# Kernel optimization log

Measured on AMD Instinct MI355X. Metric: run time of the kernel, lower is better.

The kernel has to match this reference:

```python
import jax, jax.numpy as jnp
import numpy as np

VOCAB = 38
EMB = 128
CTX = 5  # context window size
HIDDEN = [512, 256, 128]


def setup_inputs() -> dict:
    key = jax.random.key(0)
    ks = jax.random.split(key, 16)
    B, S = 64, 1024
    encrypted_input = jax.random.randint(ks[0], (B, S), 0, VOCAB, dtype=jnp.int32)
    # embedding table, uniform(-0.1, 0.1), padding_idx=0 row zeroed
    emb = jax.random.uniform(ks[1], (VOCAB, EMB), jnp.float32, -0.1, 0.1)
    emb = emb.at[0].set(0.0)
    dims = [EMB * CTX] + HIDDEN + [VOCAB]
    params = {}
    for i in range(len(dims) - 1):
        fan_in, fan_out = dims[i], dims[i + 1]
        limit = float(np.sqrt(6.0 / (fan_in + fan_out)))  # xavier uniform
        params[f"W{i+1}"] = jax.random.uniform(ks[2 + i], (fan_out, fan_in), jnp.float32, -limit, limit)
        params[f"b{i+1}"] = jnp.zeros((fan_out,), jnp.float32)
    return {"encrypted_input": encrypted_input, "emb": emb, **params}


def reference(encrypted_input, emb, W1, b1, W2, b2, W3, b3, W4, b4):
    B, S = encrypted_input.shape
    pad = CTX // 2
    x = emb[encrypted_input]                                   # [B, S, E]
    xp = jnp.pad(x, ((0, 0), (pad, pad), (0, 0)))              # [B, S+4, E]
    # sliding window of CTX tokens, flattened -> [B, S, CTX*E]
    ctx = jnp.concatenate([xp[:, i:i + S, :] for i in range(CTX)], axis=-1)
    h = ctx.reshape(B * S, CTX * EMB)                          # fused batched GEMM rows
    h = jax.nn.relu(h @ W1.T + b1)
    h = jax.nn.relu(h @ W2.T + b2)
    h = jax.nn.relu(h @ W3.T + b3)
    out = h @ W4.T + b4                                        # [B*S, VOCAB]
    return out.reshape(B, S, VOCAB)
```

## Files before the change

### kernel.cpp

```cpp
#include <hip/hip_runtime.h>
#include <hip/hip_bf16.h>

#define SEQ 1024

typedef __attribute__((ext_vector_type(8))) short s16x8;
typedef __attribute__((ext_vector_type(4))) float f32x4;
typedef __attribute__((ext_vector_type(2))) unsigned int u32x2;
typedef __attribute__((ext_vector_type(4))) unsigned int u32x4;
typedef __attribute__((ext_vector_type(2))) float f32x2;

#define P01P 0
#define G2P  (1521 * 512)
#define P34P (G2P + 39 * 512)
#define W2P  (P34P + 1521 * 512)
#define W3P  (W2P + 256 * 512)
#define W4P  (W3P + 64 * 512)
#define BF_END (W4P + 12 * 512)

#define F2 (16 * 16)
#define F3 (8 * 8)
#define F4 (3 * 4)
#define FTOT (F2 + F3 + F4)

__device__ __forceinline__ unsigned int f2bf(float f) {
    unsigned int u = __float_as_uint(f);
    return (u + 0x7fffu + ((u >> 16) & 1u)) >> 16;
}

__device__ __forceinline__ unsigned short bfbits(float f) {
    __hip_bfloat16 h = __float2bfloat16(f);
    unsigned short u;
    __builtin_memcpy(&u, &h, 2);
    return u;
}

__device__ __forceinline__ unsigned pk2(float a, float b) {
    return (unsigned)bfbits(a) | ((unsigned)bfbits(b) << 16);
}

__device__ __forceinline__ float bf2f(short x) {
    return __uint_as_float(((unsigned)(unsigned short)x) << 16);
}

__global__ void prep1(const float* __restrict__ w1, const float* __restrict__ w2,
                      const float* __restrict__ w3, const float* __restrict__ w4,
                      const float* __restrict__ emb, unsigned short* __restrict__ dst) {
    if (blockIdx.x < 195) {
        float* gf = reinterpret_cast<float*>(dst + BF_END);
        const int j = blockIdx.x / 39;
        const int v = blockIdx.x % 39;
        const int o = threadIdx.x;
        if (v >= 38) { gf[(j * 39 + v) * 512 + o] = 0.f; return; }
        __shared__ float ev[128];
        if (threadIdx.x < 128) ev[threadIdx.x] = emb[v * 128 + threadIdx.x];
        __syncthreads();
        const float* wr = w1 + o * 640 + j * 128;
        float s = 0.f;
        #pragma unroll
        for (int e = 0; e < 128; e += 4) {
            const float4 a = *reinterpret_cast<const float4*>(wr + e);
            s += a.x * ev[e] + a.y * ev[e + 1] + a.z * ev[e + 2] + a.w * ev[e + 3];
        }
        gf[(j * 39 + v) * 512 + o] = s;
    } else {
        const int g = (blockIdx.x - 195) * 512 + threadIdx.x;
        if (g >= FTOT * 64) return;
        const int lane = g & 63;
        const int t    = g >> 6;
        const float* w; int K, N, KC, base, tl;
        if (t < F2)           { w = w2; K = 512; N = 256; KC = 16; base = W2P; tl = t; }
        else if (t < F2 + F3) { w = w3; K = 256; N = 128; KC = 8;  base = W3P; tl = t - F2; }
        else                  { w = w4; K = 128; N = 38;  KC = 4;  base = W4P; tl = t - F2 - F3; }
        const int ct  = tl / KC;
        const int kc  = tl - ct * KC;
        const int col = ct * 16 + (lane & 15);
        const int k0  = kc * 32 + (lane >> 4) * 8;
        unsigned short o8[8];
        #pragma unroll
        for (int e = 0; e < 8; ++e)
            o8[e] = (col < N) ? (unsigned short)f2bf(w[col * K + k0 + e]) : (unsigned short)0;
        *reinterpret_cast<s16x8*>(dst + base + (size_t)(tl * 64 + lane) * 8) =
            *reinterpret_cast<s16x8*>(o8);
    }
}

__global__ void prep2(const float* __restrict__ b1, unsigned short* __restrict__ dst) {
    const float* gf = reinterpret_cast<const float*>(dst + BF_END);
    const int o   = threadIdx.x;
    const int bid = blockIdx.x;
    if (bid < 1521) {
        const int v0 = bid / 39, v1 = bid % 39;
        const float s = b1[o] + gf[(0 * 39 + v0) * 512 + o] + gf[(1 * 39 + v1) * 512 + o];
        dst[P01P + bid * 512 + o] = bfbits(s);
    } else if (bid < 1560) {
        const int v = bid - 1521;
        dst[G2P + v * 512 + o] = bfbits(gf[(2 * 39 + v) * 512 + o]);
    } else {
        const int p = bid - 1560;
        const int v3 = p / 39, v4 = p % 39;
        dst[P34P + p * 512 + o] = bfbits(gf[(3 * 39 + v3) * 512 + o] + gf[(4 * 39 + v4) * 512 + o]);
    }
}

#define H1S 0
#define H2S 32768
#define H3S 0

#define SWZ(b, row) ((b) ^ (((row) & 15) << 4))

__device__ __forceinline__ u32x2 pack_relu(f32x4 a, float4 b) {
    u32x2 r;
    r[0] = pk2(fmaxf(a[0] + b.x, 0.f), fmaxf(a[1] + b.y, 0.f));
    r[1] = pk2(fmaxf(a[2] + b.z, 0.f), fmaxf(a[3] + b.w, 0.f));
    return r;
}

__launch_bounds__(512, 6)
__global__ void fused_mlp(const int* __restrict__ tok,
                          const unsigned short* __restrict__ wbf,
                          const float* __restrict__ b2,
                          const float* __restrict__ b3,
                          const float* __restrict__ b4,
                          float* __restrict__ out) {
    __shared__ char smem[49152];
    const int tid  = threadIdx.x;
    const int lane = tid & 63;
    const int wave = tid >> 6;
    const int l15  = lane & 15;
    const int l4   = lane >> 4;
    const int r0   = blockIdx.x * 32;
    const int s0   = r0 & (SEQ - 1);
    const int bat  = r0 >> 10;

    int* tokL = reinterpret_cast<int*>(smem + H2S);

    if (tid < 36) {
        const int sp = s0 - 2 + tid;
        tokL[tid] = (sp >= 0 && sp < SEQ) ? tok[bat * SEQ + sp] : 38;
    }
    __syncthreads();

    {
        const int row = tid >> 4;
        const int c16 = tid & 15;
        const int t0 = tokL[row],     t1 = tokL[row + 1], t2 = tokL[row + 2];
        const int t3 = tokL[row + 3], t4 = tokL[row + 4];
        const unsigned short* pa = wbf + P01P + (t0 * 39 + t1) * 512;
        const unsigned short* pb = wbf + G2P  + t2 * 512;
        const unsigned short* pc = wbf + P34P + (t3 * 39 + t4) * 512;
        #pragma unroll
        for (int it = 0; it < 4; ++it) {
            const int c8 = it * 16 + c16;
            const s16x8 va = *reinterpret_cast<const s16x8*>(pa + c8 * 8);
            const s16x8 vb = *reinterpret_cast<const s16x8*>(pb + c8 * 8);
            const s16x8 vc = *reinterpret_cast<const s16x8*>(pc + c8 * 8);
            u32x4 wv;
            #pragma unroll
            for (int h = 0; h < 4; ++h) {
                const float e0 = bf2f(va[2 * h])     + bf2f(vb[2 * h])     + bf2f(vc[2 * h]);
                const float e1 = bf2f(va[2 * h + 1]) + bf2f(vb[2 * h + 1]) + bf2f(vc[2 * h + 1]);
                wv[h] = pk2(fmaxf(e0, 0.f), fmaxf(e1, 0.f));
            }
            *reinterpret_cast<u32x4*>(smem + H1S + SWZ(row * 1024 + c8 * 16, row)) = wv;
        }
    }
    __syncthreads();

    {
        f32x4 acc[2][2];
        #pragma unroll
        for (int rt = 0; rt < 2; ++rt)
            #pragma unroll
            for (int ct = 0; ct < 2; ++ct) acc[rt][ct] = (f32x4){0.f, 0.f, 0.f, 0.f};
        for (int ks = 0; ks < 16; ++ks) {
            s16x8 xv[2];
            #pragma unroll
            for (int rt = 0; rt < 2; ++rt) {
                const int row = rt * 16 + l15;
                xv[rt] = *reinterpret_cast<const s16x8*>(
                    smem + H1S + SWZ(row * 1024 + ks * 64 + l4 * 16, row));
            }
            #pragma unroll
            for (int ct = 0; ct < 2; ++ct) {
                const s16x8 w = *reinterpret_cast<const s16x8*>(
                    wbf + W2P + (((wave * 2 + ct) * 16 + ks) * 64 + lane) * 8);
                #pragma unroll
                for (int rt = 0; rt < 2; ++rt)
                    acc[rt][ct] = __builtin_amdgcn_mfma_f32_16x16x32_bf16(w, xv[rt], acc[rt][ct], 0, 0, 0);
            }
        }
        #pragma unroll
        for (int ct = 0; ct < 2; ++ct) {
            const int col0 = (wave * 2 + ct) * 16 + l4 * 4;
            const float4 bb = *reinterpret_cast<const float4*>(b2 + col0);
            #pragma unroll
            for (int rt = 0; rt < 2; ++rt) {
                const int row = rt * 16 + l15;
                *reinterpret_cast<u32x2*>(smem + H2S + SWZ(row * 512 + col0 * 2, row)) =
                    pack_relu(acc[rt][ct], bb);
            }
        }
    }
    __syncthreads();

    {
        f32x4 acc[2];
        #pragma unroll
        for (int rt = 0; rt < 2; ++rt) acc[rt] = (f32x4){0.f, 0.f, 0.f, 0.f};
        for (int ks = 0; ks < 8; ++ks) {
            const s16x8 w = *reinterpret_cast<const s16x8*>(
                wbf + W3P + ((wave * 8 + ks) * 64 + lane) * 8);
            #pragma unroll
            for (int rt = 0; rt < 2; ++rt) {
                const int row = rt * 16 + l15;
                const s16x8 xv = *reinterpret_cast<const s16x8*>(
                    smem + H2S + SWZ(row * 512 + ks * 64 + l4 * 16, row));
                acc[rt] = __builtin_amdgcn_mfma_f32_16x16x32_bf16(w, xv, acc[rt], 0, 0, 0);
            }
        }
        const int col0 = wave * 16 + l4 * 4;
        const float4 bb = *reinterpret_cast<const float4*>(b3 + col0);
        #pragma unroll
        for (int rt = 0; rt < 2; ++rt) {
            const int row = rt * 16 + l15;
            *reinterpret_cast<u32x2*>(smem + H3S + SWZ(row * 256 + col0 * 2, row)) =
                pack_relu(acc[rt], bb);
        }
    }
    __syncthreads();

    if (wave < 6) {
        const int rt = wave & 1;
        const int mt = wave >> 1;
        f32x4 acc = (f32x4){0.f, 0.f, 0.f, 0.f};
        #pragma unroll
        for (int ks = 0; ks < 4; ++ks) {
            const int row = rt * 16 + l15;
            const s16x8 xv = *reinterpret_cast<const s16x8*>(
                smem + H3S + SWZ(row * 256 + ks * 64 + l4 * 16, row));
            const s16x8 w = *reinterpret_cast<const s16x8*>(
                wbf + W4P + ((mt * 4 + ks) * 64 + lane) * 8);
            acc = __builtin_amdgcn_mfma_f32_16x16x32_bf16(w, xv, acc, 0, 0, 0);
        }
        const int rg   = r0 + rt * 16 + l15;
        const int col0 = mt * 16 + l4 * 4;
        #pragma unroll
        for (int h = 0; h < 2; ++h) {
            const int c = col0 + 2 * h;
            if (c < 38) {
                f32x2 v;
                v[0] = acc[2 * h]     + b4[c];
                v[1] = acc[2 * h + 1] + b4[c + 1];
                *reinterpret_cast<f32x2*>(out + rg * 38 + c) = v;
            }
        }
    }
}

extern "C" void kernel_launch(void* const* d_in, const int* in_sizes, int n_in,
                              void* d_out, int out_size, void* d_ws, size_t ws_size,
                              hipStream_t stream) {
    const int*   tok = (const int*)d_in[0];
    const float* emb = (const float*)d_in[1];
    const float* W1  = (const float*)d_in[2];
    const float* b1  = (const float*)d_in[3];
    const float* W2  = (const float*)d_in[4];
    const float* b2  = (const float*)d_in[5];
    const float* W3  = (const float*)d_in[6];
    const float* b3  = (const float*)d_in[7];
    const float* W4  = (const float*)d_in[8];
    const float* b4  = (const float*)d_in[9];
    float* out = (float*)d_out;
    unsigned short* wbf = (unsigned short*)d_ws;

    const int pack_blocks = (FTOT * 64 + 511) / 512;
    prep1<<<195 + pack_blocks, 512, 0, stream>>>(W1, W2, W3, W4, emb, wbf);
    prep2<<<1521 + 39 + 1521, 512, 0, stream>>>(b1, wbf);
    fused_mlp<<<2048, 512, 0, stream>>>(tok, wbf, b2, b3, b4, out);
}
```

Baseline: 60.59 us.

## Double rows per block and split layer-1 gather into two K-halves overlapping MFMA

The fused MLP block now handles 64 rows instead of 32, so each W2/W3/W4 weight fragment loaded from global memory feeds twice as many MFMAs. The layer-1 activation gather is split into two 256-wide halves in separate LDS buffers, so the second half's gather can overlap the first half's layer-2 MFMAs. prep2 also merges the P01 and P34 pair-table builds into one block each, which cuts its grid size. In exchange, LDS use grows to about 64.5KB, occupancy drops (launch bounds 6→4), and accumulator register pressure rises.

```diff
diff --git a/kernel.cpp b/kernel.cpp
--- a/kernel.cpp
+++ b/kernel.cpp
@@ -89,22 +89,20 @@
     const int o   = threadIdx.x;
     const int bid = blockIdx.x;
     if (bid < 1521) {
-        const int v0 = bid / 39, v1 = bid % 39;
-        const float s = b1[o] + gf[(0 * 39 + v0) * 512 + o] + gf[(1 * 39 + v1) * 512 + o];
-        dst[P01P + bid * 512 + o] = bfbits(s);
-    } else if (bid < 1560) {
+        const int va = bid / 39, vb = bid % 39;
+        dst[P01P + bid * 512 + o] =
+            bfbits(b1[o] + gf[(0 * 39 + va) * 512 + o] + gf[(1 * 39 + vb) * 512 + o]);
+        dst[P34P + bid * 512 + o] =
+            bfbits(gf[(3 * 39 + va) * 512 + o] + gf[(4 * 39 + vb) * 512 + o]);
+    } else {
         const int v = bid - 1521;
         dst[G2P + v * 512 + o] = bfbits(gf[(2 * 39 + v) * 512 + o]);
-    } else {
-        const int p = bid - 1560;
-        const int v3 = p / 39, v4 = p % 39;
-        dst[P34P + p * 512 + o] = bfbits(gf[(3 * 39 + v3) * 512 + o] + gf[(4 * 39 + v4) * 512 + o]);
-    }
-}
-
-#define H1S 0
-#define H2S 32768
-#define H3S 0
+    }
+}
+
+#define BA 0
+#define BB 32768
+#define TOKO 65536
 
 #define SWZ(b, row) ((b) ^ (((row) & 15) << 4))
 
@@ -115,45 +113,73 @@
     return r;
 }
 
-__launch_bounds__(512, 6)
+__launch_bounds__(512, 4)
 __global__ void fused_mlp(const int* __restrict__ tok,
                           const unsigned short* __restrict__ wbf,
                           const float* __restrict__ b2,
                           const float* __restrict__ b3,
                           const float* __restrict__ b4,
                           float* __restrict__ out) {
-    __shared__ char smem[49152];
+    __shared__ char smem[65536 + 512];
     const int tid  = threadIdx.x;
     const int lane = tid & 63;
     const int wave = tid >> 6;
     const int l15  = lane & 15;
     const int l4   = lane >> 4;
-    const int r0   = blockIdx.x * 32;
+    const int r0   = blockIdx.x * 64;
     const int s0   = r0 & (SEQ - 1);
     const int bat  = r0 >> 10;
 
-    int* tokL = reinterpret_cast<int*>(smem + H2S);
-
-    if (tid < 36) {
+    int* tokL = reinterpret_cast<int*>(smem + TOKO);
+
+    if (tid < 68) {
         const int sp = s0 - 2 + tid;
         tokL[tid] = (sp >= 0 && sp < SEQ) ? tok[bat * SEQ + sp] : 38;
     }
     __syncthreads();
 
+    const int p1row = tid >> 3;
+    const int p1c   = tid & 7;
+    int off01, off2, off34;
     {
-        const int row = tid >> 4;
-        const int c16 = tid & 15;
-        const int t0 = tokL[row],     t1 = tokL[row + 1], t2 = tokL[row + 2];
-        const int t3 = tokL[row + 3], t4 = tokL[row + 4];
-        const unsigned short* pa = wbf + P01P + (t0 * 39 + t1) * 512;
-        const unsigned short* pb = wbf + G2P  + t2 * 512;
-        const unsigned short* pc = wbf + P34P + (t3 * 39 + t4) * 512;
+        const int t0 = tokL[p1row],     t1 = tokL[p1row + 1], t2 = tokL[p1row + 2];
+        const int t3 = tokL[p1row + 3], t4 = tokL[p1row + 4];
+        off01 = (t0 * 39 + t1) * 512;
+        off2  = t2 * 512;
+        off34 = (t3 * 39 + t4) * 512;
+    }
+
+    #pragma unroll
+    for (int it = 0; it < 4; ++it) {
+        const int c8 = it * 8 + p1c;
+        const int d  = c8 * 8;
+        const s16x8 va = *reinterpret_cast<const s16x8*>(wbf + P01P + off01 + d);
+        const s16x8 vb = *reinterpret_cast<const s16x8*>(wbf + G2P  + off2  + d);
+        const s16x8 vc = *reinterpret_cast<const s16x8*>(wbf + P34P + off34 + d);
+        u32x4 wv;
+        #pragma unroll
+        for (int h = 0; h < 4; ++h) {
+            const float e0 = bf2f(va[2 * h])     + bf2f(vb[2 * h])     + bf2f(vc[2 * h]);
+            const float e1 = bf2f(va[2 * h + 1]) + bf2f(vb[2 * h + 1]) + bf2f(vc[2 * h + 1]);
+            wv[h] = pk2(fmaxf(e0, 0.f), fmaxf(e1, 0.f));
+        }
+        *reinterpret_cast<u32x4*>(smem + BA + SWZ(p1row * 512 + c8 * 16, p1row)) = wv;
+    }
+    __syncthreads();
+
+    f32x4 acc2[4][2];
+    #pragma unroll
+    for (int rt = 0; rt < 4; ++rt)
+        #pragma unroll
+        for (int ct = 0; ct < 2; ++ct) acc2[rt][ct] = (f32x4){0.f, 0.f, 0.f, 0.f};
+    {
         #pragma unroll
         for (int it = 0; it < 4; ++it) {
-            const int c8 = it * 16 + c16;
-            const s16x8 va = *reinterpret_cast<const s16x8*>(pa + c8 * 8);
-            const s16x8 vb = *reinterpret_cast<const s16x8*>(pb + c8 * 8);
-            const s16x8 vc = *reinterpret_cast<const s16x8*>(pc + c8 * 8);
+            const int c8 = it * 8 + p1c;
+            const int d  = 256 + c8 * 8;
+            const s16x8 va = *reinterpret_cast<const s16x8*>(wbf + P01P + off01 + d);
+            const s16x8 vb = *reinterpret_cast<const s16x8*>(wbf + G2P  + off2  + d);
+            const s16x8 vc = *reinterpret_cast<const s16x8*>(wbf + P34P + off34 + d);
             u32x4 wv;
             #pragma unroll
             for (int h = 0; h < 4; ++h) {
@@ -161,32 +187,44 @@
                 const float e1 = bf2f(va[2 * h + 1]) + bf2f(vb[2 * h + 1]) + bf2f(vc[2 * h + 1]);
                 wv[h] = pk2(fmaxf(e0, 0.f), fmaxf(e1, 0.f));
             }
-            *reinterpret_cast<u32x4*>(smem + H1S + SWZ(row * 1024 + c8 * 16, row)) = wv;
-        }
-    }
-    __syncthreads();
-
-    {
-        f32x4 acc[2][2];
-        #pragma unroll
-        for (int rt = 0; rt < 2; ++rt)
-            #pragma unroll
-            for (int ct = 0; ct < 2; ++ct) acc[rt][ct] = (f32x4){0.f, 0.f, 0.f, 0.f};
-        for (int ks = 0; ks < 16; ++ks) {
-            s16x8 xv[2];
-            #pragma unroll
-            for (int rt = 0; rt < 2; ++rt) {
+            *reinterpret_cast<u32x4*>(smem + BB + SWZ(p1row * 512 + c8 * 16, p1row)) = wv;
+        }
+        for (int ks = 0; ks < 8; ++ks) {
+            s16x8 xv[4];
+            #pragma unroll
+            for (int rt = 0; rt < 4; ++rt) {
                 const int row = rt * 16 + l15;
                 xv[rt] = *reinterpret_cast<const s16x8*>(
-                    smem + H1S + SWZ(row * 1024 + ks * 64 + l4 * 16, row));
+                    smem + BA + SWZ(row * 512 + ks * 64 + l4 * 16, row));
             }
             #pragma unroll
             for (int ct = 0; ct < 2; ++ct) {
                 const s16x8 w = *reinterpret_cast<const s16x8*>(
                     wbf + W2P + (((wave * 2 + ct) * 16 + ks) * 64 + lane) * 8);
                 #pragma unroll
-                for (int rt = 0; rt < 2; ++rt)
-                    acc[rt][ct] = __builtin_amdgcn_mfma_f32_16x16x32_bf16(w, xv[rt], acc[rt][ct], 0, 0, 0);
+                for (int rt = 0; rt < 4; ++rt)
+                    acc2[rt][ct] = __builtin_amdgcn_mfma_f32_16x16x32_bf16(w, xv[rt], acc2[rt][ct], 0, 0, 0);
+            }
+        }
+    }
+    __syncthreads();
+
+    {
+        for (int ks = 0; ks < 8; ++ks) {
+            s16x8 xv[4];
+            #pragma unroll
+            for (int rt = 0; rt < 4; ++rt) {
+                const int row = rt * 16 + l15;
+                xv[rt] = *reinterpret_cast<const s16x8*>(
+                    smem + BB + SWZ(row * 512 + ks * 64 + l4 * 16, row));
+            }
+            #pragma unroll
+            for (int ct = 0; ct < 2; ++ct) {
+                const s16x8 w = *reinterpret_cast<const s16x8*>(
+                    wbf + W2P + (((wave * 2 + ct) * 16 + 8 + ks) * 64 + lane) * 8);
+                #pragma unroll
+                for (int rt = 0; rt < 4; ++rt)
+                    acc2[rt][ct] = __builtin_amdgcn_mfma_f32_16x16x32_bf16(w, xv[rt], acc2[rt][ct], 0, 0, 0);
             }
         }
         #pragma unroll
@@ -194,50 +232,50 @@
             const int col0 = (wave * 2 + ct) * 16 + l4 * 4;
             const float4 bb = *reinterpret_cast<const float4*>(b2 + col0);
             #pragma unroll
-            for (int rt = 0; rt < 2; ++rt) {
+            for (int rt = 0; rt < 4; ++rt) {
                 const int row = rt * 16 + l15;
-                *reinterpret_cast<u32x2*>(smem + H2S + SWZ(row * 512 + col0 * 2, row)) =
-                    pack_relu(acc[rt][ct], bb);
+                *reinterpret_cast<u32x2*>(smem + BA + SWZ(row * 512 + col0 * 2, row)) =
+                    pack_relu(acc2[rt][ct], bb);
             }
         }
     }
     __syncthreads();
 
     {
-        f32x4 acc[2];
-        #pragma unroll
-        for (int rt = 0; rt < 2; ++rt) acc[rt] = (f32x4){0.f, 0.f, 0.f, 0.f};
+        f32x4 acc[4];
+        #pragma unroll
+        for (int rt = 0; rt < 4; ++rt) acc[rt] = (f32x4){0.f, 0.f, 0.f, 0.f};
         for (int ks = 0; ks < 8; ++ks) {
             const s16x8 w = *reinterpret_cast<const s16x8*>(
                 wbf + W3P + ((wave * 8 + ks) * 64 + lane) * 8);
             #pragma unroll
-            for (int rt = 0; rt < 2; ++rt) {
+            for (int rt = 0; rt < 4; ++rt) {
                 const int row = rt * 16 + l15;
                 const s16x8 xv = *reinterpret_cast<const s16x8*>(
-                    smem + H2S + SWZ(row * 512 + ks * 64 + l4 * 16, row));
+                    smem + BA + SWZ(row * 512 + ks * 64 + l4 * 16, row));
                 acc[rt] = __builtin_amdgcn_mfma_f32_16x16x32_bf16(w, xv, acc[rt], 0, 0, 0);
             }
         }
         const int col0 = wave * 16 + l4 * 4;
         const float4 bb = *reinterpret_cast<const float4*>(b3 + col0);
         #pragma unroll
-        for (int rt = 0; rt < 2; ++rt) {
+        for (int rt = 0; rt < 4; ++rt) {
             const int row = rt * 16 + l15;
-            *reinterpret_cast<u32x2*>(smem + H3S + SWZ(row * 256 + col0 * 2, row)) =
+            *reinterpret_cast<u32x2*>(smem + BB + SWZ(row * 256 + col0 * 2, row)) =
                 pack_relu(acc[rt], bb);
         }
     }
     __syncthreads();
 
-    if (wave < 6) {
-        const int rt = wave & 1;
-        const int mt = wave >> 1;
+    for (int task = wave; task < 12; task += 8) {
+        const int mt = task >> 2;
+        const int rt = task & 3;
         f32x4 acc = (f32x4){0.f, 0.f, 0.f, 0.f};
         #pragma unroll
         for (int ks = 0; ks < 4; ++ks) {
             const int row = rt * 16 + l15;
             const s16x8 xv = *reinterpret_cast<const s16x8*>(
-                smem + H3S + SWZ(row * 256 + ks * 64 + l4 * 16, row));
+                smem + BB + SWZ(row * 256 + ks * 64 + l4 * 16, row));
             const s16x8 w = *reinterpret_cast<const s16x8*>(
                 wbf + W4P + ((mt * 4 + ks) * 64 + lane) * 8);
             acc = __builtin_amdgcn_mfma_f32_16x16x32_bf16(w, xv, acc, 0, 0, 0);
@@ -275,6 +313,6 @@
 
     const int pack_blocks = (FTOT * 64 + 511) / 512;
     prep1<<<195 + pack_blocks, 512, 0, stream>>>(W1, W2, W3, W4, emb, wbf);
-    prep2<<<1521 + 39 + 1521, 512, 0, stream>>>(b1, wbf);
-    fused_mlp<<<2048, 512, 0, stream>>>(tok, wbf, b2, b3, b4, out);
-}
+    prep2<<<1521 + 39, 512, 0, stream>>>(b1, wbf);
+    fused_mlp<<<1024, 512, 0, stream>>>(tok, wbf, b2, b3, b4, out);
+}
```

Result: slower. 62.55 us (+3.2%).
